# Optimization experiments

Measured on AMD Instinct MI355X. Metric: run time of the kernel, lower is better.

The kernel has to match this reference:

```python
import jax, jax.numpy as jnp
import numpy as np

NH = 8          # num_heads (init kwarg)
NUM_GROUPS = 32
EPS = 1e-5


def setup_inputs() -> dict:
    key = jax.random.key(0)
    ks = jax.random.split(key, 4)
    B, C, H, W = 2, 512, 64, 64
    x = jax.random.normal(ks[0], (B, C, H, W), dtype=jnp.float32)
    qkv_w = jax.random.normal(ks[1], (3 * C, C), dtype=jnp.float32) * (1.0 / np.sqrt(C))
    proj_w = jax.random.normal(ks[2], (C, C), dtype=jnp.float32) * (1.0 / np.sqrt(C))
    proj_b = jax.random.normal(ks[3], (C,), dtype=jnp.float32) * 0.02
    gn_w = jnp.ones((C,), dtype=jnp.float32)
    gn_b = jnp.zeros((C,), dtype=jnp.float32)
    return {"x": x, "qkv_w": qkv_w, "proj_w": proj_w, "proj_b": proj_b,
            "gn_w": gn_w, "gn_b": gn_b}


def _group_norm(x, gamma, beta):
    B, C, H, W = x.shape
    xg = x.reshape(B, NUM_GROUPS, C // NUM_GROUPS, H, W)
    mean = xg.mean(axis=(2, 3, 4), keepdims=True)
    var = xg.var(axis=(2, 3, 4), keepdims=True)
    xg = (xg - mean) * jax.lax.rsqrt(var + EPS)
    x = xg.reshape(B, C, H, W)
    return x * gamma[None, :, None, None] + beta[None, :, None, None]


def reference(x, qkv_w, proj_w, proj_b, gn_w, gn_b):
    B, C, H, W = x.shape
    h = _group_norm(x, gn_w, gn_b)
    # 1x1 conv == channel matmul
    qkv = jnp.einsum('oc,bchw->bohw', qkv_w, h)  # [B, 3C, H, W]
    # faithful legacy reshape: per-head contiguous [q,k,v] blocks of 3*C//NH channels
    qkv = qkv.reshape(B * NH, 3 * C // NH, H * W)
    q, k, v = jnp.split(qkv, 3, axis=1)          # each [B*NH, C//NH, HW]
    scale = 1.0 / np.sqrt(np.sqrt(C // NH))
    attn = jnp.einsum('bci,bcj->bij', q * scale, k * scale)  # [B*NH, HW, HW]
    attn = jax.nn.softmax(attn, axis=-1)
    hout = jnp.einsum('bij,bcj->bci', attn, v)   # [B*NH, C//NH, HW]
    hout = hout.reshape(B, C, H, W)
    hout = jnp.einsum('oc,bchw->bohw', proj_w, hout) + proj_b[None, :, None, None]
    return x + hout
```

## Files before the change

### kernel.cpp

```cpp
#include <hip/hip_runtime.h>
#include <math.h>

typedef __attribute__((ext_vector_type(8))) short short8;
typedef __attribute__((ext_vector_type(4))) short short4v;
typedef __attribute__((ext_vector_type(4))) float floatx4;
typedef __attribute__((ext_vector_type(16))) float floatx16;

__device__ __forceinline__ unsigned short f2bf(float f) {
  union { float f; unsigned int u; } v; v.f = f;
  unsigned int r = v.u + 0x7fffu + ((v.u >> 16) & 1u);
  return (unsigned short)(r >> 16);
}

__device__ __forceinline__ float bf2f(unsigned short h) {
  union { unsigned int u; float f; } v; v.u = ((unsigned int)h) << 16;
  return v.f;
}

__device__ __forceinline__ unsigned int pack2(unsigned short a, unsigned short b) {
  return (unsigned int)a | ((unsigned int)b << 16);
}

__device__ __forceinline__ unsigned int rbits(float f) {
  union { float f; unsigned int u; } v; v.f = f;
  return v.u + 0x8000u;
}

__device__ __forceinline__ float fast_exp2(float x) {
#if __has_builtin(__builtin_amdgcn_exp2f)
  return __builtin_amdgcn_exp2f(x);
#else
  return exp2f(x);
#endif
}

__device__ __forceinline__ void async16(const unsigned short* gp, unsigned short* lp) {
  __builtin_amdgcn_global_load_lds(
      (__attribute__((address_space(1))) void*)(gp),
      (__attribute__((address_space(3))) void*)(lp), 16, 0, 0);
}

__global__ void setup_kernel(const float* __restrict__ x, float* __restrict__ stats,
                             const float* __restrict__ qkv_w, unsigned short* __restrict__ wqkv,
                             const float* __restrict__ proj_w, unsigned short* __restrict__ wproj) {
  if (blockIdx.x < 64) {
    int bg = blockIdx.x;
    const float4* p = (const float4*)(x + (size_t)bg * 65536);
    float s = 0.f, ss = 0.f;
    for (int i = threadIdx.x; i < 16384; i += 256) {
      float4 v = p[i];
      s  += v.x + v.y + v.z + v.w;
      ss += v.x*v.x + v.y*v.y + v.z*v.z + v.w*v.w;
    }
    #pragma unroll
    for (int off = 32; off >= 1; off >>= 1) {
      s  += __shfl_xor(s,  off, 64);
      ss += __shfl_xor(ss, off, 64);
    }
    __shared__ float red[2][4];
    int wv = threadIdx.x >> 6;
    if ((threadIdx.x & 63) == 0) { red[0][wv] = s; red[1][wv] = ss; }
    __syncthreads();
    if (threadIdx.x == 0) {
      s  = red[0][0] + red[0][1] + red[0][2] + red[0][3];
      ss = red[1][0] + red[1][1] + red[1][2] + red[1][3];
      float mean = s * (1.f/65536.f);
      float var  = ss * (1.f/65536.f) - mean*mean;
      stats[2*bg]   = mean;
      stats[2*bg+1] = rsqrtf(var + 1e-5f);
    }
  } else {
    int i = (blockIdx.x - 64) * 256 + threadIdx.x;
    const float* s; unsigned short* d;
    if (i < 196608) { s = qkv_w; d = wqkv; }
    else { i -= 196608; s = proj_w; d = wproj; }
    float4 vv = ((const float4*)s)[i];
    uint2 o;
    o.x = pack2(f2bf(vv.x), f2bf(vv.y));
    o.y = pack2(f2bf(vv.z), f2bf(vv.w));
    ((uint2*)d)[i] = o;
  }
}

__global__ void gn_apply_t(const float* __restrict__ x, const float* __restrict__ stats,
                           const float* __restrict__ gw, const float* __restrict__ gb,
                           unsigned short* __restrict__ h_t) {
  __shared__ __align__(16) unsigned short tile[64][72];
  const int b = blockIdx.z, c0 = blockIdx.y * 64, hw0 = blockIdx.x * 64;
  const int t = threadIdx.x;
  {
    const int cl = t >> 2;
    const int hs = (t & 3) * 16;
    const int c  = c0 + cl;
    const int g  = c >> 4;
    const float mean = stats[2*(b*32 + g)];
    const float rstd = stats[2*(b*32 + g) + 1];
    const float w  = gw[c] * rstd;
    const float bb = gb[c] - mean * w;
    const float4* src = (const float4*)(x + ((size_t)(b*512 + c))*4096 + hw0 + hs);
    #pragma unroll
    for (int i = 0; i < 4; i++) {
      float4 vv = src[i];
      unsigned short* d = &tile[cl][hs + i*4];
      d[0] = f2bf(vv.x*w + bb); d[1] = f2bf(vv.y*w + bb);
      d[2] = f2bf(vv.z*w + bb); d[3] = f2bf(vv.w*w + bb);
    }
  }
  __syncthreads();
  {
    const int hwl = t >> 2;
    const int cs  = (t & 3) * 16;
    uint4 w0, w1;
    w0.x = pack2(tile[cs+ 0][hwl], tile[cs+ 1][hwl]);
    w0.y = pack2(tile[cs+ 2][hwl], tile[cs+ 3][hwl]);
    w0.z = pack2(tile[cs+ 4][hwl], tile[cs+ 5][hwl]);
    w0.w = pack2(tile[cs+ 6][hwl], tile[cs+ 7][hwl]);
    w1.x = pack2(tile[cs+ 8][hwl], tile[cs+ 9][hwl]);
    w1.y = pack2(tile[cs+10][hwl], tile[cs+11][hwl]);
    w1.z = pack2(tile[cs+12][hwl], tile[cs+13][hwl]);
    w1.w = pack2(tile[cs+14][hwl], tile[cs+15][hwl]);
    unsigned short* dst = h_t + ((size_t)(b*4096 + hw0 + hwl))*512 + c0 + cs;
    *(uint4*)dst       = w0;
    *(uint4*)(dst + 8) = w1;
  }
}

__global__ __launch_bounds__(256, 2)
void qkv_gemm(const unsigned short* __restrict__ A,
              const unsigned short* __restrict__ Bt,
              unsigned short* __restrict__ q_t,
              unsigned short* __restrict__ k_t,
              unsigned short* __restrict__ v_) {
  __shared__ __align__(16) unsigned short As[128*32];
  __shared__ __align__(16) unsigned short Bs[128*32];
  const int b   = blockIdx.z;
  const int n0  = blockIdx.x * 128;
  const int o0  = blockIdx.y * 128;
  const int tid = threadIdx.x;
  const int wave = tid >> 6, lane = tid & 63;
  const int wr = wave >> 1, wc = wave & 1;
  const int fm = lane & 15, fq = lane >> 4;
  const int srow = lane >> 2, scol = (lane & 3) * 8;

  const unsigned short* Ab = A + (size_t)o0 * 512;
  const unsigned short* Bb = Bt + ((size_t)b*4096 + n0) * 512;

  bool vsw[4];
  #pragma unroll
  for (int fr = 0; fr < 4; fr++) {
    const int ob = o0 + wr*64 + fr*16;
    vsw[fr] = ((ob % 192) >> 6) == 2;
  }

  floatx4 acc[4][4];
  #pragma unroll
  for (int i = 0; i < 4; i++)
    #pragma unroll
    for (int j = 0; j < 4; j++) acc[i][j] = (floatx4){0.f,0.f,0.f,0.f};

  for (int k0 = 0; k0 < 512; k0 += 32) {
    __syncthreads();
    #pragma unroll
    for (int cc = 0; cc < 2; cc++) {
      int ch = wave*2 + cc;
      async16(Ab + (size_t)(ch*16 + srow)*512 + k0 + scol, &As[ch*512]);
      async16(Bb + (size_t)(ch*16 + srow)*512 + k0 + scol, &Bs[ch*512]);
    }
    __syncthreads();
    short8 af[4], bf[4];
    #pragma unroll
    for (int f = 0; f < 4; f++) {
      af[f] = *(const short8*)&As[(wr*64 + f*16 + fm)*32 + fq*8];
      bf[f] = *(const short8*)&Bs[(wc*64 + f*16 + fm)*32 + fq*8];
    }
    #pragma unroll
    for (int fr = 0; fr < 4; fr++) {
      if (vsw[fr]) {
        #pragma unroll
        for (int fc = 0; fc < 4; fc++)
          acc[fr][fc] = __builtin_amdgcn_mfma_f32_16x16x32_bf16(bf[fc], af[fr], acc[fr][fc], 0, 0, 0);
      } else {
        #pragma unroll
        for (int fc = 0; fc < 4; fc++)
          acc[fr][fc] = __builtin_amdgcn_mfma_f32_16x16x32_bf16(af[fr], bf[fc], acc[fr][fc], 0, 0, 0);
      }
    }
  }

  #pragma unroll
  for (int fr = 0; fr < 4; fr++) {
    const int ob     = o0 + wr*64 + fr*16;
    const int head   = ob / 192;
    const int rem    = ob % 192;
    const int region = rem >> 6;
    const int bhh    = b*8 + head;
    #pragma unroll
    for (int fc = 0; fc < 4; fc++) {
      if (region == 0) {
        const int i = n0 + wc*64 + fc*16 + fm;
        const int dsub = (rem & 63) + fq*4;
        unsigned short t4[4];
        #pragma unroll
        for (int r = 0; r < 4; r++) t4[r] = f2bf(acc[fr][fc][r] * 0.18033688f);
        uint2 o; o.x = pack2(t4[0], t4[1]); o.y = pack2(t4[2], t4[3]);
        *(uint2*)&q_t[((size_t)bhh*4096 + i)*64 + dsub] = o;
      } else if (region == 1) {
        const int i = n0 + wc*64 + fc*16 + fm;
        const int dsub = (rem & 63) + fq*4;
        unsigned short t4[4];
        #pragma unroll
        for (int r = 0; r < 4; r++) t4[r] = f2bf(acc[fr][fc][r]);
        uint2 o; o.x = pack2(t4[0], t4[1]); o.y = pack2(t4[2], t4[3]);
        *(uint2*)&k_t[((size_t)bhh*4096 + i)*64 + dsub] = o;
      } else {
        const int dsub = (rem & 63) + fm;
        const int tok0 = n0 + wc*64 + fc*16 + fq*4;
        unsigned short t4[4];
        #pragma unroll
        for (int r = 0; r < 4; r++) t4[r] = f2bf(acc[fr][fc][r]);
        uint2 o; o.x = pack2(t4[0], t4[1]); o.y = pack2(t4[2], t4[3]);
        *(uint2*)&v_[((size_t)bhh*64 + dsub)*4096 + tok0] = o;
      }
    }
  }
}

__global__ __launch_bounds__(256, 2)
void proj_gemm(const unsigned short* __restrict__ A,
               const unsigned short* __restrict__ Bt,
               float* __restrict__ outp,
               const float* __restrict__ xres,
               const float* __restrict__ pbias) {
  __shared__ __align__(16) unsigned short As[64*32];
  __shared__ __align__(16) unsigned short Bs[128*32];
  const int b   = blockIdx.z;
  const int n0  = blockIdx.x * 128;
  const int o0  = blockIdx.y * 64;
  const int tid = threadIdx.x;
  const int wave = tid >> 6, lane = tid & 63;
  const int wr = wave >> 1, wc = wave & 1;
  const int fm = lane & 15, fq = lane >> 4;
  const int srow = lane >> 2, scol = (lane & 3) * 8;

  const unsigned short* Ab = A + (size_t)o0 * 512;
  const unsigned short* Bb = Bt + ((size_t)b*4096 + n0) * 512;

  floatx4 acc[2][4];
  #pragma unroll
  for (int i = 0; i < 2; i++)
    #pragma unroll
    for (int j = 0; j < 4; j++) acc[i][j] = (floatx4){0.f,0.f,0.f,0.f};

  for (int k0 = 0; k0 < 512; k0 += 32) {
    __syncthreads();
    async16(Ab + (size_t)(wave*16 + srow)*512 + k0 + scol, &As[wave*512]);
    #pragma unroll
    for (int cc = 0; cc < 2; cc++) {
      int ch = wave*2 + cc;
      async16(Bb + (size_t)(ch*16 + srow)*512 + k0 + scol, &Bs[ch*512]);
    }
    __syncthreads();
    short8 af[2], bf[4];
    #pragma unroll
    for (int f = 0; f < 2; f++)
      af[f] = *(const short8*)&As[(wr*32 + f*16 + fm)*32 + fq*8];
    #pragma unroll
    for (int f = 0; f < 4; f++)
      bf[f] = *(const short8*)&Bs[(wc*64 + f*16 + fm)*32 + fq*8];
    #pragma unroll
    for (int fr = 0; fr < 2; fr++)
      #pragma unroll
      for (int fc = 0; fc < 4; fc++)
        acc[fr][fc] = __builtin_amdgcn_mfma_f32_16x16x32_bf16(af[fr], bf[fc], acc[fr][fc], 0, 0, 0);
  }

  #pragma unroll
  for (int fr = 0; fr < 2; fr++)
    #pragma unroll
    for (int fc = 0; fc < 4; fc++) {
      const int i = n0 + wc*64 + fc*16 + fm;
      #pragma unroll
      for (int r = 0; r < 4; r++) {
        const int o = o0 + wr*32 + fr*16 + fq*4 + r;
        const size_t idx = ((size_t)b*512 + o)*4096 + i;
        outp[idx] = xres[idx] + pbias[o] + acc[fr][fc][r];
      }
    }
}

template <int SPLIT>
__global__ __launch_bounds__(256, 4)
void attn_kernel(const unsigned short* __restrict__ q_t,
                 const unsigned short* __restrict__ k_t,
                 const unsigned short* __restrict__ v_,
                 unsigned short* __restrict__ hout_t,
                 unsigned short* __restrict__ o_part,
                 float* __restrict__ l_part) {
  __shared__ __align__(16) unsigned short Ks[2][64*72];
  __shared__ __align__(16) unsigned short Vs[2][64*72];

  const int bh  = blockIdx.x;
  const int q0  = blockIdx.y * 128;
  const int js  = SPLIT ? blockIdx.z : 0;
  const int nit = SPLIT ? 32 : 64;
  const int jbase = js * 2048;
  const int tid = threadIdx.x;
  const int wave = tid >> 6, lane = tid & 63;
  const int ln = lane & 31, h = lane >> 5;

  short8 qf[4];
  {
    const unsigned short* qrow = q_t + ((size_t)bh*4096 + q0 + wave*32 + ln)*64;
    #pragma unroll
    for (int kc = 0; kc < 4; kc++)
      qf[kc] = *(const short8*)(qrow + kc*16 + h*8);
  }

  const floatx16 z16 = {0.f,0.f,0.f,0.f,0.f,0.f,0.f,0.f,
                        0.f,0.f,0.f,0.f,0.f,0.f,0.f,0.f};
  floatx16 o_acc[2];
  o_acc[0] = z16; o_acc[1] = z16;
  float l = 0.f;

  const int sr = tid >> 3;
  const int sc = (tid & 7) * 8;
  const int cch = tid & 7;
  const int vpos = ((cch >> 2) * 32) + ((cch & 3) * 4);
  const unsigned short* kbase = k_t + (size_t)bh*262144;
  const unsigned short* vbase = v_  + (size_t)bh*262144;

  uint4 kr0 = *(const uint4*)&kbase[(size_t)(jbase + sr)*64 + sc];
  uint4 kr1 = *(const uint4*)&kbase[(size_t)(jbase + sr + 32)*64 + sc];
  uint4 vr0 = *(const uint4*)&vbase[(size_t)sr*4096 + jbase + sc];
  uint4 vr1 = *(const uint4*)&vbase[(size_t)(sr+32)*4096 + jbase + sc];

  for (int it = 0; it < nit; it++) {
    unsigned short* Kc = Ks[it & 1];
    unsigned short* Vc = Vs[it & 1];
    *(uint4*)&Kc[sr*72 + sc]      = kr0;
    *(uint4*)&Kc[(sr+32)*72 + sc] = kr1;
    *(uint2*)&Vc[sr*72 + vpos]           = *(const uint2*)&vr0;
    *(uint2*)&Vc[sr*72 + vpos + 16]      = *((const uint2*)&vr0 + 1);
    *(uint2*)&Vc[(sr+32)*72 + vpos]      = *(const uint2*)&vr1;
    *(uint2*)&Vc[(sr+32)*72 + vpos + 16] = *((const uint2*)&vr1 + 1);
    __syncthreads();

    {
      const int jn = jbase + (((it + 1) & (nit - 1)) * 64);
      kr0 = *(const uint4*)&kbase[(size_t)(jn + sr)*64 + sc];
      kr1 = *(const uint4*)&kbase[(size_t)(jn + sr + 32)*64 + sc];
      vr0 = *(const uint4*)&vbase[(size_t)sr*4096 + jn + sc];
      vr1 = *(const uint4*)&vbase[(size_t)(sr+32)*4096 + jn + sc];
    }

    #pragma unroll
    for (int mj = 0; mj < 2; mj++) {
      floatx16 st;
      {
        short8 kA = *(const short8*)&Kc[(mj*32 + ln)*72 + h*8];
        st = __builtin_amdgcn_mfma_f32_32x32x16_bf16(kA, qf[0], z16, 0, 0, 0);
      }
      #pragma unroll
      for (int kc = 1; kc < 4; kc++) {
        short8 kA = *(const short8*)&Kc[(mj*32 + ln)*72 + kc*16 + h*8];
        st = __builtin_amdgcn_mfma_f32_32x32x16_bf16(kA, qf[kc], st, 0, 0, 0);
      }

      unsigned pk[8];
      #pragma unroll
      for (int rp = 0; rp < 8; rp++) {
        float p0 = fast_exp2(st[2*rp]);
        float p1 = fast_exp2(st[2*rp + 1]);
        l += p0 + p1;
        pk[rp] = __builtin_amdgcn_perm(rbits(p1), rbits(p0), 0x07060302u);
      }

      #pragma unroll
      for (int t2 = 0; t2 < 2; t2++) {
        union { unsigned u[2]; short4v s; } a0, a1;
        a0.u[0] = pk[4*t2];     a0.u[1] = pk[4*t2 + 1];
        a1.u[0] = pk[4*t2 + 2]; a1.u[1] = pk[4*t2 + 3];
        #pragma unroll
        for (int dn = 0; dn < 2; dn++) {
          short8 vv = *(const short8*)&Vc[(dn*32 + ln)*72 + mj*32 + h*16 + t2*8];
          short4v vlo = __builtin_shufflevector(vv, vv, 0, 1, 2, 3);
          short4v vhi = __builtin_shufflevector(vv, vv, 4, 5, 6, 7);
          o_acc[dn] = __builtin_amdgcn_mfma_f32_32x32x8bf16_1k(a0.s, vlo, o_acc[dn], 0, 0, 0);
          o_acc[dn] = __builtin_amdgcn_mfma_f32_32x32x8bf16_1k(a1.s, vhi, o_acc[dn], 0, 0, 0);
        }
      }
    }
  }

  l += __shfl_xor(l, 32, 64);

  if (SPLIT) {
    unsigned short* op = o_part + (((size_t)(js*16 + bh)*4096 + q0 + wave*32) * 64);
    #pragma unroll
    for (int r = 0; r < 16; r++) {
      const int il = (r & 3) + 8*(r >> 2) + 4*h;
      op[(size_t)il*64 + ln]      = f2bf(o_acc[0][r]);
      op[(size_t)il*64 + 32 + ln] = f2bf(o_acc[1][r]);
    }
    if (lane < 32)
      l_part[(size_t)(js*16 + bh)*4096 + q0 + wave*32 + lane] = l;
  } else {
    const float linv = 1.f / l;
    const int bb = bh >> 3;
    const int cb = (bh & 7) * 64;
    #pragma unroll
    for (int r = 0; r < 16; r++) {
      const int il = (r & 3) + 8*(r >> 2) + 4*h;
      const float inv = __shfl(linv, il, 64);
      const int i = q0 + wave*32 + il;
      unsigned short* dst = &hout_t[((size_t)bb*4096 + i)*512 + cb + ln];
      dst[0]  = f2bf(o_acc[0][r] * inv);
      dst[32] = f2bf(o_acc[1][r] * inv);
    }
  }
}

__global__ void attn_combine(const unsigned short* __restrict__ o_part,
                             const float* __restrict__ l_part,
                             unsigned short* __restrict__ hout_t) {
  const int bh = blockIdx.x;
  const int i0 = blockIdx.y * 64;
  const int t  = threadIdx.x;
  const int d4 = (t & 15) * 4;
  const int il = t >> 4;
  const int bb = bh >> 3;
  const int cb = (bh & 7) * 64;
  const size_t JS = (size_t)16 * 4096 * 64;
  #pragma unroll
  for (int p = 0; p < 4; p++) {
    const int i = i0 + p*16 + il;
    const size_t ob = ((size_t)bh*4096 + i)*64 + d4;
    uint2 a = *(const uint2*)&o_part[ob];
    uint2 b = *(const uint2*)&o_part[ob + JS];
    const size_t lb = (size_t)bh*4096 + i;
    const float inv = 1.f / (l_part[lb] + l_part[lb + 65536]);
    float o0 = (bf2f((unsigned short)(a.x & 0xffff)) + bf2f((unsigned short)(b.x & 0xffff))) * inv;
    float o1 = (bf2f((unsigned short)(a.x >> 16))    + bf2f((unsigned short)(b.x >> 16)))    * inv;
    float o2 = (bf2f((unsigned short)(a.y & 0xffff)) + bf2f((unsigned short)(b.y & 0xffff))) * inv;
    float o3 = (bf2f((unsigned short)(a.y >> 16))    + bf2f((unsigned short)(b.y >> 16)))    * inv;
    uint2 w;
    w.x = pack2(f2bf(o0), f2bf(o1));
    w.y = pack2(f2bf(o2), f2bf(o3));
    *(uint2*)&hout_t[((size_t)bb*4096 + i)*512 + cb + d4] = w;
  }
}

extern "C" void kernel_launch(void* const* d_in, const int* in_sizes, int n_in,
                              void* d_out, int out_size, void* d_ws, size_t ws_size,
                              hipStream_t stream) {
  (void)in_sizes; (void)n_in; (void)out_size;
  const float* x      = (const float*)d_in[0];
  const float* qkv_w  = (const float*)d_in[1];
  const float* proj_w = (const float*)d_in[2];
  const float* proj_b = (const float*)d_in[3];
  const float* gn_w   = (const float*)d_in[4];
  const float* gn_b   = (const float*)d_in[5];
  float* out = (float*)d_out;

  char* ws = (char*)d_ws;
  unsigned short* h_t   = (unsigned short*)(ws);
  unsigned short* q_t   = (unsigned short*)(ws + ((size_t)8  << 20));
  unsigned short* k_t   = (unsigned short*)(ws + ((size_t)16 << 20));
  unsigned short* v_    = (unsigned short*)(ws + ((size_t)24 << 20));
  unsigned short* wqkv  = (unsigned short*)(ws + ((size_t)32 << 20));
  unsigned short* wproj = (unsigned short*)(ws + ((size_t)34 << 20));
  float* stats          = (float*)(ws + ((size_t)35 << 20));
  unsigned short* o_part = (unsigned short*)(ws + ((size_t)36 << 20));
  float* l_part          = (float*)(ws + ((size_t)52 << 20));
  unsigned short* hout_t = h_t;

  const bool split = ws_size >= (((size_t)52 << 20) + ((size_t)1 << 19));

  setup_kernel<<<dim3(1088), dim3(256), 0, stream>>>(x, stats, qkv_w, wqkv, proj_w, wproj);
  gn_apply_t<<<dim3(64, 8, 2), dim3(256), 0, stream>>>(x, stats, gn_w, gn_b, h_t);
  qkv_gemm<<<dim3(32, 12, 2), dim3(256), 0, stream>>>(wqkv, h_t, q_t, k_t, v_);
  if (split) {
    attn_kernel<1><<<dim3(16, 32, 2), dim3(256), 0, stream>>>(q_t, k_t, v_, nullptr,
                                                              o_part, l_part);
    attn_combine<<<dim3(16, 64), dim3(256), 0, stream>>>(o_part, l_part, hout_t);
  } else {
    attn_kernel<0><<<dim3(16, 32), dim3(256), 0, stream>>>(q_t, k_t, v_, hout_t,
                                                           nullptr, nullptr);
  }
  proj_gemm<<<dim3(32, 8, 2), dim3(256), 0, stream>>>(wproj, hout_t, out, x, proj_b);
}
```

Before: 234.7 us.

## Double query rows per attention wave to reuse K/V fragments

Each attention wave now handles 64 query rows as two 32-row halves instead of one, with the query tile per block growing to 256. K and V fragments loaded from LDS are reused across both halves, halving LDS reads and global K/V tile loads per query. The grid shrinks to half as many blocks, and more accumulators raise register pressure, so launch bounds drop to 2 blocks per SM. The qkv_gemm launch-bounds occupancy hint is also raised from 2 to 3.

```diff
diff --git a/kernel.cpp b/kernel.cpp
--- a/kernel.cpp
+++ b/kernel.cpp
@@ -125,7 +125,7 @@
   }
 }
 
-__global__ __launch_bounds__(256, 2)
+__global__ __launch_bounds__(256, 3)
 void qkv_gemm(const unsigned short* __restrict__ A,
               const unsigned short* __restrict__ Bt,
               unsigned short* __restrict__ q_t,
@@ -289,7 +289,7 @@
 }
 
 template <int SPLIT>
-__global__ __launch_bounds__(256, 4)
+__global__ __launch_bounds__(256, 2)
 void attn_kernel(const unsigned short* __restrict__ q_t,
                  const unsigned short* __restrict__ k_t,
                  const unsigned short* __restrict__ v_,
@@ -300,7 +300,7 @@
   __shared__ __align__(16) unsigned short Vs[2][64*72];
 
   const int bh  = blockIdx.x;
-  const int q0  = blockIdx.y * 128;
+  const int q0  = blockIdx.y * 256;
   const int js  = SPLIT ? blockIdx.z : 0;
   const int nit = SPLIT ? 32 : 64;
   const int jbase = js * 2048;
@@ -308,19 +308,21 @@
   const int wave = tid >> 6, lane = tid & 63;
   const int ln = lane & 31, h = lane >> 5;
 
-  short8 qf[4];
-  {
-    const unsigned short* qrow = q_t + ((size_t)bh*4096 + q0 + wave*32 + ln)*64;
+  short8 qf[2][4];
+  #pragma unroll
+  for (int ih = 0; ih < 2; ih++) {
+    const unsigned short* qrow = q_t + ((size_t)bh*4096 + q0 + wave*64 + ih*32 + ln)*64;
     #pragma unroll
     for (int kc = 0; kc < 4; kc++)
-      qf[kc] = *(const short8*)(qrow + kc*16 + h*8);
+      qf[ih][kc] = *(const short8*)(qrow + kc*16 + h*8);
   }
 
   const floatx16 z16 = {0.f,0.f,0.f,0.f,0.f,0.f,0.f,0.f,
                         0.f,0.f,0.f,0.f,0.f,0.f,0.f,0.f};
-  floatx16 o_acc[2];
-  o_acc[0] = z16; o_acc[1] = z16;
-  float l = 0.f;
+  floatx16 o_acc[2][2];
+  #pragma unroll
+  for (int ih = 0; ih < 2; ih++) { o_acc[ih][0] = z16; o_acc[ih][1] = z16; }
+  float l0 = 0.f, l1 = 0.f;
 
   const int sr = tid >> 3;
   const int sc = (tid & 7) * 8;
@@ -355,67 +357,87 @@
 
     #pragma unroll
     for (int mj = 0; mj < 2; mj++) {
-      floatx16 st;
-      {
-        short8 kA = *(const short8*)&Kc[(mj*32 + ln)*72 + h*8];
-        st = __builtin_amdgcn_mfma_f32_32x32x16_bf16(kA, qf[0], z16, 0, 0, 0);
-      }
-      #pragma unroll
-      for (int kc = 1; kc < 4; kc++) {
-        short8 kA = *(const short8*)&Kc[(mj*32 + ln)*72 + kc*16 + h*8];
-        st = __builtin_amdgcn_mfma_f32_32x32x16_bf16(kA, qf[kc], st, 0, 0, 0);
-      }
-
-      unsigned pk[8];
-      #pragma unroll
-      for (int rp = 0; rp < 8; rp++) {
-        float p0 = fast_exp2(st[2*rp]);
-        float p1 = fast_exp2(st[2*rp + 1]);
-        l += p0 + p1;
-        pk[rp] = __builtin_amdgcn_perm(rbits(p1), rbits(p0), 0x07060302u);
-      }
-
-      #pragma unroll
-      for (int t2 = 0; t2 < 2; t2++) {
-        union { unsigned u[2]; short4v s; } a0, a1;
-        a0.u[0] = pk[4*t2];     a0.u[1] = pk[4*t2 + 1];
-        a1.u[0] = pk[4*t2 + 2]; a1.u[1] = pk[4*t2 + 3];
-        #pragma unroll
-        for (int dn = 0; dn < 2; dn++) {
-          short8 vv = *(const short8*)&Vc[(dn*32 + ln)*72 + mj*32 + h*16 + t2*8];
-          short4v vlo = __builtin_shufflevector(vv, vv, 0, 1, 2, 3);
-          short4v vhi = __builtin_shufflevector(vv, vv, 4, 5, 6, 7);
-          o_acc[dn] = __builtin_amdgcn_mfma_f32_32x32x8bf16_1k(a0.s, vlo, o_acc[dn], 0, 0, 0);
-          o_acc[dn] = __builtin_amdgcn_mfma_f32_32x32x8bf16_1k(a1.s, vhi, o_acc[dn], 0, 0, 0);
+      short8 kf[4];
+      #pragma unroll
+      for (int kc = 0; kc < 4; kc++)
+        kf[kc] = *(const short8*)&Kc[(mj*32 + ln)*72 + kc*16 + h*8];
+      short8 vv[2][2];
+      #pragma unroll
+      for (int dn = 0; dn < 2; dn++)
+        #pragma unroll
+        for (int t2 = 0; t2 < 2; t2++)
+          vv[dn][t2] = *(const short8*)&Vc[(dn*32 + ln)*72 + mj*32 + h*16 + t2*8];
+
+      #pragma unroll
+      for (int ih = 0; ih < 2; ih++) {
+        floatx16 st = __builtin_amdgcn_mfma_f32_32x32x16_bf16(kf[0], qf[ih][0], z16, 0, 0, 0);
+        #pragma unroll
+        for (int kc = 1; kc < 4; kc++)
+          st = __builtin_amdgcn_mfma_f32_32x32x16_bf16(kf[kc], qf[ih][kc], st, 0, 0, 0);
+
+        unsigned pk[8];
+        float lacc = 0.f;
+        #pragma unroll
+        for (int rp = 0; rp < 8; rp++) {
+          float p0 = fast_exp2(st[2*rp]);
+          float p1 = fast_exp2(st[2*rp + 1]);
+          lacc += p0 + p1;
+          pk[rp] = __builtin_amdgcn_perm(rbits(p1), rbits(p0), 0x07060302u);
+        }
+        if (ih) l1 += lacc; else l0 += lacc;
+
+        #pragma unroll
+        for (int t2 = 0; t2 < 2; t2++) {
+          union { unsigned u[2]; short4v s; } a0, a1;
+          a0.u[0] = pk[4*t2];     a0.u[1] = pk[4*t2 + 1];
+          a1.u[0] = pk[4*t2 + 2]; a1.u[1] = pk[4*t2 + 3];
+          #pragma unroll
+          for (int dn = 0; dn < 2; dn++) {
+            short4v vlo = __builtin_shufflevector(vv[dn][t2], vv[dn][t2], 0, 1, 2, 3);
+            short4v vhi = __builtin_shufflevector(vv[dn][t2], vv[dn][t2], 4, 5, 6, 7);
+            o_acc[ih][dn] = __builtin_amdgcn_mfma_f32_32x32x8bf16_1k(a0.s, vlo, o_acc[ih][dn], 0, 0, 0);
+            o_acc[ih][dn] = __builtin_amdgcn_mfma_f32_32x32x8bf16_1k(a1.s, vhi, o_acc[ih][dn], 0, 0, 0);
+          }
         }
       }
     }
   }
 
-  l += __shfl_xor(l, 32, 64);
+  l0 += __shfl_xor(l0, 32, 64);
+  l1 += __shfl_xor(l1, 32, 64);
 
   if (SPLIT) {
-    unsigned short* op = o_part + (((size_t)(js*16 + bh)*4096 + q0 + wave*32) * 64);
-    #pragma unroll
-    for (int r = 0; r < 16; r++) {
-      const int il = (r & 3) + 8*(r >> 2) + 4*h;
-      op[(size_t)il*64 + ln]      = f2bf(o_acc[0][r]);
-      op[(size_t)il*64 + 32 + ln] = f2bf(o_acc[1][r]);
-    }
-    if (lane < 32)
-      l_part[(size_t)(js*16 + bh)*4096 + q0 + wave*32 + lane] = l;
+    #pragma unroll
+    for (int ih = 0; ih < 2; ih++) {
+      unsigned short* op = o_part +
+          (((size_t)(js*16 + bh)*4096 + q0 + wave*64 + ih*32) * 64);
+      #pragma unroll
+      for (int r = 0; r < 16; r++) {
+        const int il = (r & 3) + 8*(r >> 2) + 4*h;
+        op[(size_t)il*64 + ln]      = f2bf(o_acc[ih][0][r]);
+        op[(size_t)il*64 + 32 + ln] = f2bf(o_acc[ih][1][r]);
+      }
+    }
+    if (lane < 32) {
+      l_part[(size_t)(js*16 + bh)*4096 + q0 + wave*64 + lane]      = l0;
+      l_part[(size_t)(js*16 + bh)*4096 + q0 + wave*64 + 32 + lane] = l1;
+    }
   } else {
-    const float linv = 1.f / l;
+    const float linv0 = 1.f / l0;
+    const float linv1 = 1.f / l1;
     const int bb = bh >> 3;
     const int cb = (bh & 7) * 64;
     #pragma unroll
-    for (int r = 0; r < 16; r++) {
-      const int il = (r & 3) + 8*(r >> 2) + 4*h;
-      const float inv = __shfl(linv, il, 64);
-      const int i = q0 + wave*32 + il;
-      unsigned short* dst = &hout_t[((size_t)bb*4096 + i)*512 + cb + ln];
-      dst[0]  = f2bf(o_acc[0][r] * inv);
-      dst[32] = f2bf(o_acc[1][r] * inv);
+    for (int ih = 0; ih < 2; ih++) {
+      #pragma unroll
+      for (int r = 0; r < 16; r++) {
+        const int il = (r & 3) + 8*(r >> 2) + 4*h;
+        const float inv = __shfl(ih ? linv1 : linv0, il, 64);
+        const int i = q0 + wave*64 + ih*32 + il;
+        unsigned short* dst = &hout_t[((size_t)bb*4096 + i)*512 + cb + ln];
+        dst[0]  = f2bf(o_acc[ih][0][r] * inv);
+        dst[32] = f2bf(o_acc[ih][1][r] * inv);
+      }
     }
   }
 }
@@ -480,11 +502,11 @@
   gn_apply_t<<<dim3(64, 8, 2), dim3(256), 0, stream>>>(x, stats, gn_w, gn_b, h_t);
   qkv_gemm<<<dim3(32, 12, 2), dim3(256), 0, stream>>>(wqkv, h_t, q_t, k_t, v_);
   if (split) {
-    attn_kernel<1><<<dim3(16, 32, 2), dim3(256), 0, stream>>>(q_t, k_t, v_, nullptr,
+    attn_kernel<1><<<dim3(16, 16, 2), dim3(256), 0, stream>>>(q_t, k_t, v_, nullptr,
                                                               o_part, l_part);
     attn_combine<<<dim3(16, 64), dim3(256), 0, stream>>>(o_part, l_part, hout_t);
   } else {
-    attn_kernel<0><<<dim3(16, 32), dim3(256), 0, stream>>>(q_t, k_t, v_, hout_t,
+    attn_kernel<0><<<dim3(16, 16), dim3(256), 0, stream>>>(q_t, k_t, v_, hout_t,
                                                            nullptr, nullptr);
   }
   proj_gemm<<<dim3(32, 8, 2), dim3(256), 0, stream>>>(wproj, hout_t, out, x, proj_b);
```

New measurement: 227.1 us. 3.2% less time.
